# Kernel optimization log

Measured on AMD Instinct MI355X. Metric: run time of the kernel, lower is better.

## Reference

```python
import jax, jax.numpy as jnp
import numpy as np

EPS = 1e-5
DN = ('NCHW', 'OIHW', 'NCHW')


def ternarize(w):
    """Ternary Weight Network quantization with straight-through estimator.
    delta = 0.7 * mean|w|; alpha = mean of |w| over kept entries.
    """
    aw = jnp.abs(w)
    delta = 0.7 * aw.mean()
    mask = (aw > delta).astype(w.dtype)
    alpha = (aw * mask).sum() / jnp.maximum(mask.sum(), 1.0)
    q = alpha * jnp.sign(w) * mask
    return w + jax.lax.stop_gradient(q - w)


def bn(y, g, b, m, v):
    scale = (g / jnp.sqrt(v + EPS))[None, :, None, None]
    shift = (b - m * g / jnp.sqrt(v + EPS))[None, :, None, None]
    return y * scale + shift


def relu6(y):
    return jnp.clip(y, 0.0, 6.0)


def conv(x, w, stride=1, padding='VALID'):
    return jax.lax.conv_general_dilated(
        x, w, window_strides=(stride, stride), padding=padding,
        dimension_numbers=DN)


def setup_inputs() -> dict:
    key = jax.random.key(0)
    ks = jax.random.split(key, 16)
    inp, oup, expand = 32, 32, 6
    hidden = inp * expand  # 192
    B, H, W = 16, 112, 112
    d = {}
    d['x'] = jax.random.normal(ks[0], (B, inp, H, W), dtype=jnp.float32)
    # 1x1 expand conv
    d['w1'] = jax.random.normal(ks[1], (hidden, inp, 1, 1), dtype=jnp.float32) * 0.1
    d['g1'] = 1.0 + 0.1 * jax.random.normal(ks[2], (hidden,), dtype=jnp.float32)
    d['b1'] = 0.1 * jax.random.normal(ks[3], (hidden,), dtype=jnp.float32)
    d['m1'] = 0.1 * jax.random.normal(ks[4], (hidden,), dtype=jnp.float32)
    d['v1'] = jax.random.uniform(ks[5], (hidden,), minval=0.5, maxval=1.5, dtype=jnp.float32)
    # 3x3 dense conv (no groups in the source -> dense, not depthwise)
    d['w2'] = jax.random.normal(ks[6], (hidden, hidden, 3, 3), dtype=jnp.float32) * 0.05
    d['g2'] = 1.0 + 0.1 * jax.random.normal(ks[7], (hidden,), dtype=jnp.float32)
    d['b2'] = 0.1 * jax.random.normal(ks[8], (hidden,), dtype=jnp.float32)
    d['m2'] = 0.1 * jax.random.normal(ks[9], (hidden,), dtype=jnp.float32)
    d['v2'] = jax.random.uniform(ks[10], (hidden,), minval=0.5, maxval=1.5, dtype=jnp.float32)
    # 1x1 project conv
    d['w3'] = jax.random.normal(ks[11], (oup, hidden, 1, 1), dtype=jnp.float32) * 0.1
    d['g3'] = 1.0 + 0.1 * jax.random.normal(ks[12], (oup,), dtype=jnp.float32)
    d['b3'] = 0.1 * jax.random.normal(ks[13], (oup,), dtype=jnp.float32)
    d['m3'] = 0.1 * jax.random.normal(ks[14], (oup,), dtype=jnp.float32)
    d['v3'] = jax.random.uniform(ks[15], (oup,), minval=0.5, maxval=1.5, dtype=jnp.float32)
    return d


def reference(x, w1, g1, b1, m1, v1, w2, g2, b2, m2, v2, w3, g3, b3, m3, v3):
    # expand: 1x1 ternary conv -> BN -> ReLU6
    h = relu6(bn(conv(x, ternarize(w1)), g1, b1, m1, v1))
    # 3x3 ternary conv (stride=1, padding=1) -> BN -> ReLU6
    h = relu6(bn(conv(h, ternarize(w2), stride=1, padding=((1, 1), (1, 1))), g2, b2, m2, v2))
    # project: 1x1 ternary conv -> BN (no activation)
    h = bn(conv(h, ternarize(w3)), g3, b3, m3, v3)
    # residual connection (stride==1 and inp==oup)
    return x + h
```

## Files before the change

kernel.cpp:

```cpp
#include <hip/hip_runtime.h>


typedef __bf16 bf16x8 __attribute__((ext_vector_type(8)));
typedef __bf16 bf16x4 __attribute__((ext_vector_type(4)));
typedef float  f32x4  __attribute__((ext_vector_type(4)));

#define EPSBN 1e-5f

__device__ __forceinline__ void glds16(const void* g, void* l) {
  __builtin_amdgcn_global_load_lds(
      (const __attribute__((address_space(1))) void*)g,
      (__attribute__((address_space(3))) void*)l, 16, 0, 0);
}

__device__ __forceinline__ __bf16 tern(float w, float delta) {
  float aw = fabsf(w);
  float q = (aw > delta) ? ((w > 0.0f) ? 1.0f : -1.0f) : 0.0f;
  return (__bf16)q;
}


__global__ void stats_pass1(const float* __restrict__ w1, const float* __restrict__ w2,
                            const float* __restrict__ w3, double* __restrict__ pa) {
  __shared__ double red[256];
  int b = blockIdx.x, tid = threadIdx.x;
  int tix = b >> 5, slice = b & 31;
  const float* w = (tix == 0) ? w1 : (tix == 1) ? w2 : w3;
  int len = (tix == 1) ? 331776 : 6144;
  int per = len >> 5;
  int start = slice * per, end = start + per;
  double s = 0.0;
  for (int i = start + tid; i < end; i += 256) s += (double)fabsf(w[i]);
  red[tid] = s; __syncthreads();
  for (int off = 128; off > 0; off >>= 1) {
    if (tid < off) red[tid] += red[tid + off];
    __syncthreads();
  }
  if (tid == 0) pa[b] = red[0];
}

__global__ void stats_pass2(const float* __restrict__ w1, const float* __restrict__ w2,
                            const float* __restrict__ w3, const double* __restrict__ pa,
                            double* __restrict__ ps2, double* __restrict__ pc2) {
  __shared__ double red[256];
  int b = blockIdx.x, tid = threadIdx.x;
  int tix = b >> 5, slice = b & 31;
  const float* w = (tix == 0) ? w1 : (tix == 1) ? w2 : w3;
  int len = (tix == 1) ? 331776 : 6144;
  double tot = 0.0;
  for (int k = 0; k < 32; ++k) tot += pa[tix * 32 + k];
  float delta = 0.7f * (float)(tot / (double)len);
  int per = len >> 5;
  int start = slice * per, end = start + per;
  double s2 = 0.0, c2 = 0.0;
  for (int i = start + tid; i < end; i += 256) {
    float aw = fabsf(w[i]);
    if (aw > delta) { s2 += (double)aw; c2 += 1.0; }
  }
  red[tid] = s2; __syncthreads();
  for (int off = 128; off > 0; off >>= 1) {
    if (tid < off) red[tid] += red[tid + off];
    __syncthreads();
  }
  if (tid == 0) ps2[b] = red[0];
  __syncthreads();
  red[tid] = c2; __syncthreads();
  for (int off = 128; off > 0; off >>= 1) {
    if (tid < off) red[tid] += red[tid + off];
    __syncthreads();
  }
  if (tid == 0) pc2[b] = red[0];
}

__global__ void stats_pass3(const double* __restrict__ pa, const double* __restrict__ ps2,
                            const double* __restrict__ pc2, float* __restrict__ stats) {
  int tix = blockIdx.x;
  if (threadIdx.x != 0) return;
  double tot = 0.0, s2 = 0.0, c2 = 0.0;
  for (int k = 0; k < 32; ++k) {
    tot += pa[tix * 32 + k];
    s2  += ps2[tix * 32 + k];
    c2  += pc2[tix * 32 + k];
  }
  int len = (tix == 1) ? 331776 : 6144;
  stats[tix * 2]     = 0.7f * (float)(tot / (double)len);
  stats[tix * 2 + 1] = (float)(s2 / fmax(c2, 1.0));
}

__global__ void pack_kernel(
    const float* __restrict__ w1, const float* __restrict__ w2, const float* __restrict__ w3,
    const float* __restrict__ g1, const float* __restrict__ b1, const float* __restrict__ m1, const float* __restrict__ v1,
    const float* __restrict__ g2, const float* __restrict__ b2, const float* __restrict__ m2, const float* __restrict__ v2,
    const float* __restrict__ g3, const float* __restrict__ b3, const float* __restrict__ m3, const float* __restrict__ v3,
    const float* __restrict__ stats,
    __bf16* __restrict__ w1p, __bf16* __restrict__ w2p, __bf16* __restrict__ w3p,
    float* __restrict__ sc1, float* __restrict__ sh1,
    float* __restrict__ sc2, float* __restrict__ sh2,
    float* __restrict__ sc3, float* __restrict__ sh3) {
  int idx = blockIdx.x * 256 + threadIdx.x;
  if (idx < 331776) {
    float delta2 = stats[2];
    int c = idx / 6144, rem = idx - c * 6144;
    int co = rem >> 5, r5 = rem & 31;
    int cp = r5 >> 3, lo = r5 & 7;
    int tap = c / 6, cb = c - tap * 6;
    int ci = ((cp ^ ((co >> 2) & 3)) << 3) | lo;
    int cifull = cb * 32 + ci;
    w2p[idx] = tern(w2[(co * 192 + cifull) * 9 + tap], delta2);
    return;
  }
  idx -= 331776;
  if (idx < 6144) {
    int co = idx >> 5, c = (idx >> 3) & 3, lo = idx & 7;
    int ci = ((c ^ ((co >> 2) & 3)) << 3) | lo;
    w1p[idx] = tern(w1[co * 32 + ci], stats[0]);
    return;
  }
  idx -= 6144;
  if (idx < 6144) {
    int kc = idx >> 11, rem = idx & 2047;
    int co = rem >> 6, c = (rem >> 3) & 7, lo = rem & 7;
    int ci = ((c ^ (co & 7)) << 3) | lo;
    w3p[idx] = tern(w3[co * 192 + kc * 64 + ci], stats[4]);
    return;
  }
  idx -= 6144;
  if (idx < 192) {
    float rs = rsqrtf(v1[idx] + EPSBN);
    sc1[idx] = g1[idx] * rs * stats[1];
    sh1[idx] = b1[idx] - m1[idx] * g1[idx] * rs;
    return;
  }
  idx -= 192;
  if (idx < 192) {
    float rs = rsqrtf(v2[idx] + EPSBN);
    sc2[idx] = g2[idx] * rs * stats[3];
    sh2[idx] = b2[idx] - m2[idx] * g2[idx] * rs;
    return;
  }
  idx -= 192;
  if (idx < 32) {
    float rs = rsqrtf(v3[idx] + EPSBN);
    sc3[idx] = g3[idx] * rs * stats[5];
    sh3[idx] = b3[idx] - m3[idx] * g3[idx] * rs;
  }
}

__global__ __launch_bounds__(256)
void conv1_kernel(const float* __restrict__ x, const __bf16* __restrict__ w1p,
                  const float* __restrict__ scale1, const float* __restrict__ shift1,
                  __bf16* __restrict__ h1p) {
  __shared__ __bf16 smA[112 * 32];
  __shared__ __bf16 smB[192 * 32];
  int tid = threadIdx.x, lane = tid & 63, wave = tid >> 6;
  int h = blockIdx.x, n = blockIdx.y;

  for (int t = wave; t < 12; t += 4)
    glds16((const char*)w1p + t * 1024 + lane * 16, (char*)smB + t * 1024);

  const float* xrow = x + (long)n * 401408 + h * 112;
  for (int i = 0; i < 14; ++i) {
    int f = i * 256 + tid;
    int ci = f / 112, w = f - ci * 112;
    int col = ((ci >> 3) ^ ((w >> 2) & 3));
    smA[w * 32 + (col << 3) + (ci & 7)] = (__bf16)xrow[ci * 12544 + w];
  }
  __syncthreads();

  int mrow = lane & 15, quad = lane >> 4;
  int col16 = (quad ^ ((mrow >> 2) & 3)) * 16;
  int c0 = wave * 48;

  bf16x8 aw[3], bv[7];
#pragma unroll
  for (int ic = 0; ic < 3; ++ic)
    aw[ic] = *(const bf16x8*)((const char*)smB + (c0 + ic * 16 + mrow) * 64 + col16);
#pragma unroll
  for (int jp = 0; jp < 7; ++jp)
    bv[jp] = *(const bf16x8*)((const char*)smA + (jp * 16 + mrow) * 64 + col16);

  f32x4 acc[7][3];
#pragma unroll
  for (int jp = 0; jp < 7; ++jp)
#pragma unroll
    for (int ic = 0; ic < 3; ++ic) acc[jp][ic] = (f32x4)0.0f;

#pragma unroll
  for (int jp = 0; jp < 7; ++jp)
#pragma unroll
    for (int ic = 0; ic < 3; ++ic)
      acc[jp][ic] = __builtin_amdgcn_mfma_f32_16x16x32_bf16(aw[ic], bv[jp], acc[jp][ic], 0, 0, 0);

  __bf16* obase = h1p + ((long)(n * 114 + h + 1) * 114 + 1) * 192;
#pragma unroll
  for (int ic = 0; ic < 3; ++ic) {
    int co0 = c0 + ic * 16 + quad * 4;
    float4 sc = *(const float4*)(scale1 + co0);
    float4 sh = *(const float4*)(shift1 + co0);
#pragma unroll
    for (int jp = 0; jp < 7; ++jp) {
      int w = jp * 16 + mrow;
      bf16x4 o;
      o[0] = (__bf16)fminf(fmaxf(acc[jp][ic][0] * sc.x + sh.x, 0.0f), 6.0f);
      o[1] = (__bf16)fminf(fmaxf(acc[jp][ic][1] * sc.y + sh.y, 0.0f), 6.0f);
      o[2] = (__bf16)fminf(fmaxf(acc[jp][ic][2] * sc.z + sh.z, 0.0f), 6.0f);
      o[3] = (__bf16)fminf(fmaxf(acc[jp][ic][3] * sc.w + sh.w, 0.0f), 6.0f);
      *(bf16x4*)(obase + w * 192 + co0) = o;
    }
  }

  float4 z = make_float4(0.f, 0.f, 0.f, 0.f);
  if (tid < 48) {
    int px = (tid < 24) ? 0 : 113;
    int c8 = (tid < 24) ? tid : tid - 24;
    *(float4*)((char*)h1p + ((long)((n * 114 + h + 1) * 114 + px) * 384) + c8 * 16) = z;
  }
  if (h == 0) {
    for (int c = tid; c < 2736; c += 256)
      *(float4*)((char*)h1p + (long)(n * 114) * 114 * 384 + c * 16) = z;
  }
  if (h == 111) {
    for (int c = tid; c < 2736; c += 256)
      *(float4*)((char*)h1p + (long)(n * 114 + 113) * 114 * 384 + c * 16) = z;
  }
}


#define STAGE_W(TAP, CB, B) do {                                              \
  _Pragma("unroll")                                                           \
  for (int it_ = 0; it_ < 3; ++it_) {                                         \
    int t_ = wave + it_ * 4;                                                  \
    glds16(w2b + (long)((TAP) * 6 + (CB)) * 12288 + t_ * 1024 + lane * 16,    \
           smBb + (B) * 12288 + t_ * 1024);                                   \
  }                                                                           \
} while (0)

#define STAGE_A(CB) do {                                                      \
  _Pragma("unroll")                                                           \
  for (int it_ = 0; it_ < 8; ++it_)                                           \
    if (aoff[it_] >= 0)                                                       \
      glds16(h1b + aoff[it_] + (CB) * 64, smAb + (wave + it_ * 4) * 1024);    \
} while (0)

__global__ __launch_bounds__(256, 2)
void conv2_kernel(const __bf16* __restrict__ h1p, const __bf16* __restrict__ w2p,
                  const float* __restrict__ scale2, const float* __restrict__ shift2,
                  const __bf16* __restrict__ w3p,
                  const float* __restrict__ scale3, const float* __restrict__ shift3,
                  const float* __restrict__ x, float* __restrict__ out) {
  __shared__ __align__(16) char smem[78336];
  char* smAb = smem;
  char* smBb = smem + 29184;
  char* Pb   = smem;
  char* w3l  = smem + 43008;
  int tid = threadIdx.x, lane = tid & 63, wave = tid >> 6;
  int bh = blockIdx.x, n = blockIdx.y;
  int h0 = bh * 2;

  int aoff[8];
#pragma unroll
  for (int it = 0; it < 8; ++it) {
    int t = wave + it * 4;
    int s = t * 64 + lane;
    if (s < 1824) {
      int q = s >> 2, c = s & 3;
      int q_log = c ^ ((q >> 2) & 3);
      int prow = q / 114, pcol = q - prow * 114;
      aoff[it] = ((n * 114 + h0 + prow) * 114 + pcol) * 384 + q_log * 16;
    } else {
      aoff[it] = -1;
    }
  }

  int pg = wave >> 1, cg = wave & 1;
  int mrow = lane & 15, quad = lane >> 4;
  int col16 = (quad ^ ((mrow >> 2) & 3)) * 16;
  const char* h1b = (const char*)h1p;
  const char* w2b = (const char*)w2p;

  f32x4 acc[7][6];
#pragma unroll
  for (int jp = 0; jp < 7; ++jp)
#pragma unroll
    for (int ic = 0; ic < 6; ++ic) acc[jp][ic] = (f32x4)0.0f;

  STAGE_A(0);
  STAGE_W(0, 0, 0);
  STAGE_W(1, 0, 1);

  for (int cb = 0; cb < 6; ++cb) {
#pragma unroll
    for (int tap = 0; tap < 9; ++tap) {
      if (tap <= 6) {
        STAGE_W(tap + 2, cb, (tap + 2) & 3);
        asm volatile("s_waitcnt vmcnt(6)" ::: "memory");
      } else if (tap == 7) {
        asm volatile("s_waitcnt vmcnt(3)" ::: "memory");
      } else {
        asm volatile("s_waitcnt vmcnt(0)" ::: "memory");
      }
      __builtin_amdgcn_s_barrier();
      __builtin_amdgcn_sched_barrier(0);

      const char* bbuf = smBb + (tap & 3) * 12288;
      bf16x8 aw[6];
#pragma unroll
      for (int ic = 0; ic < 6; ++ic)
        aw[ic] = *(const bf16x8*)(bbuf + (cg * 96 + ic * 16 + mrow) * 64 + col16);

      int dy = tap / 3, dx = tap - dy * 3;
      int base = (pg + dy) * 114 + dx;
      __builtin_amdgcn_s_setprio(1);
#pragma unroll
      for (int jp = 0; jp < 7; ++jp) {
        int row = base + jp * 16 + mrow;
        bf16x8 av = *(const bf16x8*)(smAb + row * 64 +
                                     ((quad ^ ((row >> 2) & 3)) * 16));
#pragma unroll
        for (int ic = 0; ic < 6; ++ic)
          acc[jp][ic] = __builtin_amdgcn_mfma_f32_16x16x32_bf16(aw[ic], av, acc[jp][ic], 0, 0, 0);
      }
      __builtin_amdgcn_s_setprio(0);
    }

    if (cb < 5) {
      asm volatile("s_waitcnt lgkmcnt(0)" ::: "memory");
      __builtin_amdgcn_sched_barrier(0);
      __builtin_amdgcn_s_barrier();
      STAGE_A(cb + 1);
      STAGE_W(0, cb + 1, 0);
      STAGE_W(1, cb + 1, 1);
    }
  }

  asm volatile("s_waitcnt lgkmcnt(0)" ::: "memory");
  __builtin_amdgcn_s_barrier();
  __builtin_amdgcn_sched_barrier(0);

#pragma unroll
  for (int it = 0; it < 3; ++it) {
    int t = wave + it * 4;
    glds16((const char*)w3p + t * 1024 + lane * 16, w3l + t * 1024);
  }

  int cohalf = wave & 1;
  int co3 = cohalf * 16 + mrow;
  float sc3v = scale3[co3], sh3v = shift3[co3];
  int fbase = (wave >> 1) * 4;

#pragma unroll
  for (int rg = 0; rg < 2; ++rg) {
    if (pg == rg) {
#pragma unroll
      for (int ic = 0; ic < 6; ++ic) {
        int co0 = cg * 96 + ic * 16 + quad * 4;
        float4 sc = *(const float4*)(scale2 + co0);
        float4 sh = *(const float4*)(shift2 + co0);
        int kc = co0 >> 6, c6 = co0 & 63;
        int chunk = c6 >> 3, off = c6 & 7;
#pragma unroll
        for (int jp = 0; jp < 7; ++jp) {
          int px = jp * 16 + mrow;
          bf16x4 o;
          o[0] = (__bf16)fminf(fmaxf(acc[jp][ic][0] * sc.x + sh.x, 0.0f), 6.0f);
          o[1] = (__bf16)fminf(fmaxf(acc[jp][ic][1] * sc.y + sh.y, 0.0f), 6.0f);
          o[2] = (__bf16)fminf(fmaxf(acc[jp][ic][2] * sc.z + sh.z, 0.0f), 6.0f);
          o[3] = (__bf16)fminf(fmaxf(acc[jp][ic][3] * sc.w + sh.w, 0.0f), 6.0f);
          *(bf16x4*)(Pb + px * 384 + kc * 128 + ((chunk ^ (px & 7)) * 16) + off * 2) = o;
        }
      }
    }
    if (rg == 0)
      asm volatile("s_waitcnt vmcnt(0) lgkmcnt(0)" ::: "memory");
    else
      asm volatile("s_waitcnt lgkmcnt(0)" ::: "memory");
    __builtin_amdgcn_s_barrier();
    __builtin_amdgcn_sched_barrier(0);

    f32x4 acc3[4];
#pragma unroll
    for (int f = 0; f < 4; ++f) acc3[f] = (f32x4)0.0f;
    int swz = mrow & 7;
#pragma unroll
    for (int kc = 0; kc < 3; ++kc) {
      bf16x8 b0 = *(const bf16x8*)(w3l + kc * 4096 + (cohalf * 16 + mrow) * 128 +
                                   ((quad ^ swz) * 16));
      bf16x8 b1 = *(const bf16x8*)(w3l + kc * 4096 + (cohalf * 16 + mrow) * 128 +
                                   (((4 + quad) ^ swz) * 16));
#pragma unroll
      for (int f = 0; f < 4; ++f) {
        if (fbase + f < 7) {
          int pr = (fbase + f) * 16 + mrow;
          bf16x8 a0 = *(const bf16x8*)(Pb + pr * 384 + kc * 128 + ((quad ^ swz) * 16));
          bf16x8 a1 = *(const bf16x8*)(Pb + pr * 384 + kc * 128 + (((4 + quad) ^ swz) * 16));
          acc3[f] = __builtin_amdgcn_mfma_f32_16x16x32_bf16(a0, b0, acc3[f], 0, 0, 0);
          acc3[f] = __builtin_amdgcn_mfma_f32_16x16x32_bf16(a1, b1, acc3[f], 0, 0, 0);
        }
      }
    }
    int h = h0 + rg;
    long obase = ((long)(n * 32 + co3) * 112 + h) * 112;
    const float* xb = x + obase;
    float* ob = out + obase;
#pragma unroll
    for (int f = 0; f < 4; ++f) {
      if (fbase + f < 7) {
        int w0 = (fbase + f) * 16 + quad * 4;
        float4 xv = *(const float4*)(xb + w0);
        float4 o;
        o.x = acc3[f][0] * sc3v + sh3v + xv.x;
        o.y = acc3[f][1] * sc3v + sh3v + xv.y;
        o.z = acc3[f][2] * sc3v + sh3v + xv.z;
        o.w = acc3[f][3] * sc3v + sh3v + xv.w;
        *(float4*)(ob + w0) = o;
      }
    }
    if (rg == 0) {
      asm volatile("s_waitcnt lgkmcnt(0)" ::: "memory");
      __builtin_amdgcn_s_barrier();
      __builtin_amdgcn_sched_barrier(0);
    }
  }
}

extern "C" void kernel_launch(void* const* d_in, const int* in_sizes, int n_in,
                              void* d_out, int out_size, void* d_ws, size_t ws_size,
                              hipStream_t stream) {
  const float* x  = (const float*)d_in[0];
  const float* w1 = (const float*)d_in[1];
  const float* g1 = (const float*)d_in[2];
  const float* b1 = (const float*)d_in[3];
  const float* m1 = (const float*)d_in[4];
  const float* v1 = (const float*)d_in[5];
  const float* w2 = (const float*)d_in[6];
  const float* g2 = (const float*)d_in[7];
  const float* b2 = (const float*)d_in[8];
  const float* m2 = (const float*)d_in[9];
  const float* v2 = (const float*)d_in[10];
  const float* w3 = (const float*)d_in[11];
  const float* g3 = (const float*)d_in[12];
  const float* b3 = (const float*)d_in[13];
  const float* m3 = (const float*)d_in[14];
  const float* v3 = (const float*)d_in[15];
  float* out = (float*)d_out;

  char* ws = (char*)d_ws;
  float*  stats = (float*)ws;
  double* pa    = (double*)(ws + 256);
  double* ps2   = (double*)(ws + 1024);
  double* pc2   = (double*)(ws + 1792);
  float* sc1 = (float*)(ws + 2560);
  float* sh1 = (float*)(ws + 3328);
  float* sc2 = (float*)(ws + 4096);
  float* sh2 = (float*)(ws + 4864);
  float* sc3 = (float*)(ws + 5632);
  float* sh3 = (float*)(ws + 5760);
  __bf16* w1p = (__bf16*)(ws + 8192);
  __bf16* w3p = (__bf16*)(ws + 20480);
  __bf16* w2p = (__bf16*)(ws + 32768);
  __bf16* h1p = (__bf16*)(ws + (1 << 20));

  hipLaunchKernelGGL(stats_pass1, dim3(96), dim3(256), 0, stream, w1, w2, w3, pa);
  hipLaunchKernelGGL(stats_pass2, dim3(96), dim3(256), 0, stream, w1, w2, w3, pa, ps2, pc2);
  hipLaunchKernelGGL(stats_pass3, dim3(3), dim3(64), 0, stream, pa, ps2, pc2, stats);
  hipLaunchKernelGGL(pack_kernel, dim3(1346), dim3(256), 0, stream, w1, w2, w3,
                     g1, b1, m1, v1, g2, b2, m2, v2, g3, b3, m3, v3, stats,
                     w1p, w2p, w3p, sc1, sh1, sc2, sh2, sc3, sh3);
  hipLaunchKernelGGL(conv1_kernel, dim3(112, 16), dim3(256), 0, stream, x, w1p, sc1, sh1, h1p);
  hipLaunchKernelGGL(conv2_kernel, dim3(56, 16), dim3(256), 0, stream, h1p, w2p, sc2, sh2,
                     w3p, sc3, sh3, x, out);
}
```

Measured before the change: 267.1 us.

## Fuse expand conv into 3x3 conv kernel, recomputing halo rows in LDS

```diff
diff --git a/kernel.cpp b/kernel.cpp
--- a/kernel.cpp
+++ b/kernel.cpp
@@ -6,6 +6,13 @@
 typedef float  f32x4  __attribute__((ext_vector_type(4)));
 
 #define EPSBN 1e-5f
+
+#define XB_OFF   0
+#define W1L_OFF  43008
+#define SMA_OFF  55296
+#define SMB_OFF  99072
+#define SC1_OFF  148224
+#define SH1_OFF  148992
 
 __device__ __forceinline__ void glds16(const void* g, void* l) {
   __builtin_amdgcn_global_load_lds(
@@ -72,34 +79,34 @@
   if (tid == 0) pc2[b] = red[0];
 }
 
-__global__ void stats_pass3(const double* __restrict__ pa, const double* __restrict__ ps2,
-                            const double* __restrict__ pc2, float* __restrict__ stats) {
-  int tix = blockIdx.x;
-  if (threadIdx.x != 0) return;
-  double tot = 0.0, s2 = 0.0, c2 = 0.0;
-  for (int k = 0; k < 32; ++k) {
-    tot += pa[tix * 32 + k];
-    s2  += ps2[tix * 32 + k];
-    c2  += pc2[tix * 32 + k];
-  }
-  int len = (tix == 1) ? 331776 : 6144;
-  stats[tix * 2]     = 0.7f * (float)(tot / (double)len);
-  stats[tix * 2 + 1] = (float)(s2 / fmax(c2, 1.0));
-}
-
 __global__ void pack_kernel(
     const float* __restrict__ w1, const float* __restrict__ w2, const float* __restrict__ w3,
     const float* __restrict__ g1, const float* __restrict__ b1, const float* __restrict__ m1, const float* __restrict__ v1,
     const float* __restrict__ g2, const float* __restrict__ b2, const float* __restrict__ m2, const float* __restrict__ v2,
     const float* __restrict__ g3, const float* __restrict__ b3, const float* __restrict__ m3, const float* __restrict__ v3,
-    const float* __restrict__ stats,
+    const double* __restrict__ pa, const double* __restrict__ ps2, const double* __restrict__ pc2,
     __bf16* __restrict__ w1p, __bf16* __restrict__ w2p, __bf16* __restrict__ w3p,
     float* __restrict__ sc1, float* __restrict__ sh1,
     float* __restrict__ sc2, float* __restrict__ sh2,
     float* __restrict__ sc3, float* __restrict__ sh3) {
-  int idx = blockIdx.x * 256 + threadIdx.x;
+  __shared__ float sst[6];
+  int tid = threadIdx.x;
+  if (tid < 3) {
+    double tot = 0.0, s2 = 0.0, c2 = 0.0;
+    for (int k = 0; k < 32; ++k) {
+      tot += pa[tid * 32 + k];
+      s2  += ps2[tid * 32 + k];
+      c2  += pc2[tid * 32 + k];
+    }
+    int len = (tid == 1) ? 331776 : 6144;
+    sst[tid * 2]     = 0.7f * (float)(tot / (double)len);
+    sst[tid * 2 + 1] = (float)(s2 / fmax(c2, 1.0));
+  }
+  __syncthreads();
+
+  int idx = blockIdx.x * 256 + tid;
   if (idx < 331776) {
-    float delta2 = stats[2];
+    float delta2 = sst[2];
     int c = idx / 6144, rem = idx - c * 6144;
     int co = rem >> 5, r5 = rem & 31;
     int cp = r5 >> 3, lo = r5 & 7;
@@ -113,7 +120,7 @@
   if (idx < 6144) {
     int co = idx >> 5, c = (idx >> 3) & 3, lo = idx & 7;
     int ci = ((c ^ ((co >> 2) & 3)) << 3) | lo;
-    w1p[idx] = tern(w1[co * 32 + ci], stats[0]);
+    w1p[idx] = tern(w1[co * 32 + ci], sst[0]);
     return;
   }
   idx -= 6144;
@@ -121,188 +128,158 @@
     int kc = idx >> 11, rem = idx & 2047;
     int co = rem >> 6, c = (rem >> 3) & 7, lo = rem & 7;
     int ci = ((c ^ (co & 7)) << 3) | lo;
-    w3p[idx] = tern(w3[co * 192 + kc * 64 + ci], stats[4]);
+    w3p[idx] = tern(w3[co * 192 + kc * 64 + ci], sst[4]);
     return;
   }
   idx -= 6144;
   if (idx < 192) {
     float rs = rsqrtf(v1[idx] + EPSBN);
-    sc1[idx] = g1[idx] * rs * stats[1];
+    sc1[idx] = g1[idx] * rs * sst[1];
     sh1[idx] = b1[idx] - m1[idx] * g1[idx] * rs;
     return;
   }
   idx -= 192;
   if (idx < 192) {
     float rs = rsqrtf(v2[idx] + EPSBN);
-    sc2[idx] = g2[idx] * rs * stats[3];
+    sc2[idx] = g2[idx] * rs * sst[3];
     sh2[idx] = b2[idx] - m2[idx] * g2[idx] * rs;
     return;
   }
   idx -= 192;
   if (idx < 32) {
     float rs = rsqrtf(v3[idx] + EPSBN);
-    sc3[idx] = g3[idx] * rs * stats[5];
+    sc3[idx] = g3[idx] * rs * sst[5];
     sh3[idx] = b3[idx] - m3[idx] * g3[idx] * rs;
-  }
-}
-
-__global__ __launch_bounds__(256)
-void conv1_kernel(const float* __restrict__ x, const __bf16* __restrict__ w1p,
-                  const float* __restrict__ scale1, const float* __restrict__ shift1,
-                  __bf16* __restrict__ h1p) {
-  __shared__ __bf16 smA[112 * 32];
-  __shared__ __bf16 smB[192 * 32];
-  int tid = threadIdx.x, lane = tid & 63, wave = tid >> 6;
-  int h = blockIdx.x, n = blockIdx.y;
-
-  for (int t = wave; t < 12; t += 4)
-    glds16((const char*)w1p + t * 1024 + lane * 16, (char*)smB + t * 1024);
-
-  const float* xrow = x + (long)n * 401408 + h * 112;
-  for (int i = 0; i < 14; ++i) {
-    int f = i * 256 + tid;
-    int ci = f / 112, w = f - ci * 112;
-    int col = ((ci >> 3) ^ ((w >> 2) & 3));
-    smA[w * 32 + (col << 3) + (ci & 7)] = (__bf16)xrow[ci * 12544 + w];
-  }
-  __syncthreads();
-
-  int mrow = lane & 15, quad = lane >> 4;
-  int col16 = (quad ^ ((mrow >> 2) & 3)) * 16;
-  int c0 = wave * 48;
-
-  bf16x8 aw[3], bv[7];
-#pragma unroll
-  for (int ic = 0; ic < 3; ++ic)
-    aw[ic] = *(const bf16x8*)((const char*)smB + (c0 + ic * 16 + mrow) * 64 + col16);
-#pragma unroll
-  for (int jp = 0; jp < 7; ++jp)
-    bv[jp] = *(const bf16x8*)((const char*)smA + (jp * 16 + mrow) * 64 + col16);
-
-  f32x4 acc[7][3];
-#pragma unroll
-  for (int jp = 0; jp < 7; ++jp)
-#pragma unroll
-    for (int ic = 0; ic < 3; ++ic) acc[jp][ic] = (f32x4)0.0f;
-
-#pragma unroll
-  for (int jp = 0; jp < 7; ++jp)
-#pragma unroll
-    for (int ic = 0; ic < 3; ++ic)
-      acc[jp][ic] = __builtin_amdgcn_mfma_f32_16x16x32_bf16(aw[ic], bv[jp], acc[jp][ic], 0, 0, 0);
-
-  __bf16* obase = h1p + ((long)(n * 114 + h + 1) * 114 + 1) * 192;
-#pragma unroll
-  for (int ic = 0; ic < 3; ++ic) {
-    int co0 = c0 + ic * 16 + quad * 4;
-    float4 sc = *(const float4*)(scale1 + co0);
-    float4 sh = *(const float4*)(shift1 + co0);
-#pragma unroll
-    for (int jp = 0; jp < 7; ++jp) {
-      int w = jp * 16 + mrow;
-      bf16x4 o;
-      o[0] = (__bf16)fminf(fmaxf(acc[jp][ic][0] * sc.x + sh.x, 0.0f), 6.0f);
-      o[1] = (__bf16)fminf(fmaxf(acc[jp][ic][1] * sc.y + sh.y, 0.0f), 6.0f);
-      o[2] = (__bf16)fminf(fmaxf(acc[jp][ic][2] * sc.z + sh.z, 0.0f), 6.0f);
-      o[3] = (__bf16)fminf(fmaxf(acc[jp][ic][3] * sc.w + sh.w, 0.0f), 6.0f);
-      *(bf16x4*)(obase + w * 192 + co0) = o;
-    }
-  }
-
-  float4 z = make_float4(0.f, 0.f, 0.f, 0.f);
-  if (tid < 48) {
-    int px = (tid < 24) ? 0 : 113;
-    int c8 = (tid < 24) ? tid : tid - 24;
-    *(float4*)((char*)h1p + ((long)((n * 114 + h + 1) * 114 + px) * 384) + c8 * 16) = z;
-  }
-  if (h == 0) {
-    for (int c = tid; c < 2736; c += 256)
-      *(float4*)((char*)h1p + (long)(n * 114) * 114 * 384 + c * 16) = z;
-  }
-  if (h == 111) {
-    for (int c = tid; c < 2736; c += 256)
-      *(float4*)((char*)h1p + (long)(n * 114 + 113) * 114 * 384 + c * 16) = z;
   }
 }
 
 
 #define STAGE_W(TAP, CB, B) do {                                              \
   _Pragma("unroll")                                                           \
-  for (int it_ = 0; it_ < 3; ++it_) {                                         \
-    int t_ = wave + it_ * 4;                                                  \
-    glds16(w2b + (long)((TAP) * 6 + (CB)) * 12288 + t_ * 1024 + lane * 16,    \
-           smBb + (B) * 12288 + t_ * 1024);                                   \
+  for (int it_ = 0; it_ < 2; ++it_) {                                         \
+    int t_ = wave + it_ * 8;                                                  \
+    if (t_ < 12)                                                              \
+      glds16(w2b + (long)((TAP) * 6 + (CB)) * 12288 + t_ * 1024 + lane * 16,  \
+             smem + SMB_OFF + (B) * 12288 + t_ * 1024);                       \
   }                                                                           \
 } while (0)
 
-#define STAGE_A(CB) do {                                                      \
+#define CONV1_PHASE(CB) do {                                                  \
+  int co0_ = (CB) * 32 + cg * 16 + quad * 4;                                  \
+  float4 sc_ = *(const float4*)(smem + SC1_OFF + co0_ * 4);                   \
+  float4 sh_ = *(const float4*)(smem + SH1_OFF + co0_ * 4);                   \
+  bf16x8 aw1_ = *(const bf16x8*)(smem + W1L_OFF +                             \
+                                 ((CB) * 32 + cg * 16 + mrow) * 64 + col16);  \
   _Pragma("unroll")                                                           \
-  for (int it_ = 0; it_ < 8; ++it_)                                           \
-    if (aoff[it_] >= 0)                                                       \
-      glds16(h1b + aoff[it_] + (CB) * 64, smAb + (wave + it_ * 4) * 1024);    \
+  for (int k_ = 0; k_ < 11; ++k_) {                                           \
+    int pf_ = pg + k_ * 4;                                                    \
+    if (pf_ < 42) {                                                           \
+      int r_ = pf_ / 7;                                                       \
+      int xr_ = h0 - 1 + r_;                                                  \
+      if (xr_ >= 0 && xr_ < 112) {                                            \
+        bf16x8 bx_ = *(const bf16x8*)(smem + XB_OFF +                         \
+                                      (pf_ * 16 + mrow) * 64 + col16);        \
+        f32x4 a1_ = __builtin_amdgcn_mfma_f32_16x16x32_bf16(                  \
+            aw1_, bx_, (f32x4)0.0f, 0, 0, 0);                                 \
+        int wcol_ = (pf_ - r_ * 7) * 16 + mrow;                               \
+        int srow_ = r_ * 114 + wcol_ + 1;                                     \
+        bf16x4 o_;                                                            \
+        o_[0] = (__bf16)fminf(fmaxf(a1_[0] * sc_.x + sh_.x, 0.0f), 6.0f);     \
+        o_[1] = (__bf16)fminf(fmaxf(a1_[1] * sc_.y + sh_.y, 0.0f), 6.0f);     \
+        o_[2] = (__bf16)fminf(fmaxf(a1_[2] * sc_.z + sh_.z, 0.0f), 6.0f);     \
+        o_[3] = (__bf16)fminf(fmaxf(a1_[3] * sc_.w + sh_.w, 0.0f), 6.0f);     \
+        int chk_ = ((cg * 2 + (quad >> 1)) ^ ((srow_ >> 2) & 3)) << 4;        \
+        *(bf16x4*)(smem + SMA_OFF + srow_ * 64 + chk_ + (quad & 1) * 8) = o_; \
+      }                                                                       \
+    }                                                                         \
+  }                                                                           \
 } while (0)
 
-__global__ __launch_bounds__(256, 2)
-void conv2_kernel(const __bf16* __restrict__ h1p, const __bf16* __restrict__ w2p,
+__global__ __launch_bounds__(512, 2)
+void fused_kernel(const float* __restrict__ x, const __bf16* __restrict__ w1p,
+                  const float* __restrict__ sc1g, const float* __restrict__ sh1g,
+                  const __bf16* __restrict__ w2p,
                   const float* __restrict__ scale2, const float* __restrict__ shift2,
                   const __bf16* __restrict__ w3p,
                   const float* __restrict__ scale3, const float* __restrict__ shift3,
-                  const float* __restrict__ x, float* __restrict__ out) {
-  __shared__ __align__(16) char smem[78336];
-  char* smAb = smem;
-  char* smBb = smem + 29184;
-  char* Pb   = smem;
-  char* w3l  = smem + 43008;
+                  float* __restrict__ out) {
+  __shared__ __align__(16) char smem[149760];
   int tid = threadIdx.x, lane = tid & 63, wave = tid >> 6;
   int bh = blockIdx.x, n = blockIdx.y;
-  int h0 = bh * 2;
-
-  int aoff[8];
-#pragma unroll
-  for (int it = 0; it < 8; ++it) {
-    int t = wave + it * 4;
-    int s = t * 64 + lane;
-    if (s < 1824) {
-      int q = s >> 2, c = s & 3;
-      int q_log = c ^ ((q >> 2) & 3);
-      int prow = q / 114, pcol = q - prow * 114;
-      aoff[it] = ((n * 114 + h0 + prow) * 114 + pcol) * 384 + q_log * 16;
-    } else {
-      aoff[it] = -1;
-    }
-  }
-
+  int h0 = bh * 4;
   int pg = wave >> 1, cg = wave & 1;
   int mrow = lane & 15, quad = lane >> 4;
   int col16 = (quad ^ ((mrow >> 2) & 3)) * 16;
-  const char* h1b = (const char*)h1p;
   const char* w2b = (const char*)w2p;
 
+  for (int t = tid; t < 2736; t += 512)
+    *(float4*)(smem + SMA_OFF + t * 16) = make_float4(0.f, 0.f, 0.f, 0.f);
+
+#pragma unroll
+  for (int it = 0; it < 2; ++it) {
+    int t = wave + it * 8;
+    if (t < 12)
+      glds16((const char*)w1p + t * 1024 + lane * 16, smem + W1L_OFF + t * 1024);
+  }
+  if (tid < 192) {
+    *(float*)(smem + SC1_OFF + tid * 4) = sc1g[tid];
+    *(float*)(smem + SH1_OFF + tid * 4) = sh1g[tid];
+  }
+  {
+    const float* xn = x + (long)n * 401408;
+    for (int i = 0; i < 11; ++i) {
+      int f4 = i * 512 + tid;
+      if (f4 < 5376) {
+        int ci = f4 / 168, rem = f4 - ci * 168;
+        int px0 = rem * 4;
+        int r = px0 / 112, w0 = px0 - r * 112;
+        int xr = h0 - 1 + r;
+        if (xr >= 0 && xr < 112) {
+          float4 v = *(const float4*)(xn + (ci * 112 + xr) * 112 + w0);
+          int chunk = ((ci >> 3) ^ ((px0 >> 2) & 3)) << 4;
+          char* base = smem + XB_OFF + px0 * 64 + chunk + (ci & 7) * 2;
+          *(__bf16*)(base)       = (__bf16)v.x;
+          *(__bf16*)(base + 64)  = (__bf16)v.y;
+          *(__bf16*)(base + 128) = (__bf16)v.z;
+          *(__bf16*)(base + 192) = (__bf16)v.w;
+        }
+      }
+    }
+  }
+  asm volatile("s_waitcnt vmcnt(0) lgkmcnt(0)" ::: "memory");
+  __builtin_amdgcn_s_barrier();
+  __builtin_amdgcn_sched_barrier(0);
+
   f32x4 acc[7][6];
 #pragma unroll
   for (int jp = 0; jp < 7; ++jp)
 #pragma unroll
     for (int ic = 0; ic < 6; ++ic) acc[jp][ic] = (f32x4)0.0f;
 
-  STAGE_A(0);
   STAGE_W(0, 0, 0);
   STAGE_W(1, 0, 1);
+  CONV1_PHASE(0);
+  asm volatile("s_waitcnt lgkmcnt(0)" ::: "memory");
+  __builtin_amdgcn_s_barrier();
+  __builtin_amdgcn_sched_barrier(0);
 
   for (int cb = 0; cb < 6; ++cb) {
 #pragma unroll
     for (int tap = 0; tap < 9; ++tap) {
       if (tap <= 6) {
         STAGE_W(tap + 2, cb, (tap + 2) & 3);
-        asm volatile("s_waitcnt vmcnt(6)" ::: "memory");
+        if (wave < 4) asm volatile("s_waitcnt vmcnt(4)" ::: "memory");
+        else          asm volatile("s_waitcnt vmcnt(2)" ::: "memory");
       } else if (tap == 7) {
-        asm volatile("s_waitcnt vmcnt(3)" ::: "memory");
+        if (wave < 4) asm volatile("s_waitcnt vmcnt(2)" ::: "memory");
+        else          asm volatile("s_waitcnt vmcnt(1)" ::: "memory");
       } else {
         asm volatile("s_waitcnt vmcnt(0)" ::: "memory");
       }
       __builtin_amdgcn_s_barrier();
       __builtin_amdgcn_sched_barrier(0);
 
-      const char* bbuf = smBb + (tap & 3) * 12288;
+      const char* bbuf = smem + SMB_OFF + (tap & 3) * 12288;
       bf16x8 aw[6];
 #pragma unroll
       for (int ic = 0; ic < 6; ++ic)
@@ -314,7 +291,7 @@
 #pragma unroll
       for (int jp = 0; jp < 7; ++jp) {
         int row = base + jp * 16 + mrow;
-        bf16x8 av = *(const bf16x8*)(smAb + row * 64 +
+        bf16x8 av = *(const bf16x8*)(smem + SMA_OFF + row * 64 +
                                      ((quad ^ ((row >> 2) & 3)) * 16));
 #pragma unroll
         for (int ic = 0; ic < 6; ++ic)
@@ -327,9 +304,12 @@
       asm volatile("s_waitcnt lgkmcnt(0)" ::: "memory");
       __builtin_amdgcn_sched_barrier(0);
       __builtin_amdgcn_s_barrier();
-      STAGE_A(cb + 1);
       STAGE_W(0, cb + 1, 0);
       STAGE_W(1, cb + 1, 1);
+      CONV1_PHASE(cb + 1);
+      asm volatile("s_waitcnt lgkmcnt(0)" ::: "memory");
+      __builtin_amdgcn_s_barrier();
+      __builtin_amdgcn_sched_barrier(0);
     }
   }
 
@@ -338,18 +318,17 @@
   __builtin_amdgcn_sched_barrier(0);
 
 #pragma unroll
-  for (int it = 0; it < 3; ++it) {
-    int t = wave + it * 4;
-    glds16((const char*)w3p + t * 1024 + lane * 16, w3l + t * 1024);
-  }
-
-  int cohalf = wave & 1;
-  int co3 = cohalf * 16 + mrow;
+  for (int it = 0; it < 2; ++it) {
+    int t = wave + it * 8;
+    if (t < 12)
+      glds16((const char*)w3p + t * 1024 + lane * 16, smem + W1L_OFF + t * 1024);
+  }
+
+  int co3 = cg * 16 + mrow;
   float sc3v = scale3[co3], sh3v = shift3[co3];
-  int fbase = (wave >> 1) * 4;
-
-#pragma unroll
-  for (int rg = 0; rg < 2; ++rg) {
+
+#pragma unroll
+  for (int rg = 0; rg < 4; ++rg) {
     if (pg == rg) {
 #pragma unroll
       for (int ic = 0; ic < 6; ++ic) {
@@ -366,7 +345,8 @@
           o[1] = (__bf16)fminf(fmaxf(acc[jp][ic][1] * sc.y + sh.y, 0.0f), 6.0f);
           o[2] = (__bf16)fminf(fmaxf(acc[jp][ic][2] * sc.z + sh.z, 0.0f), 6.0f);
           o[3] = (__bf16)fminf(fmaxf(acc[jp][ic][3] * sc.w + sh.w, 0.0f), 6.0f);
-          *(bf16x4*)(Pb + px * 384 + kc * 128 + ((chunk ^ (px & 7)) * 16) + off * 2) = o;
+          *(bf16x4*)(smem + XB_OFF + px * 384 + kc * 128 +
+                     ((chunk ^ (px & 7)) * 16) + off * 2) = o;
         }
       }
     }
@@ -377,24 +357,26 @@
     __builtin_amdgcn_s_barrier();
     __builtin_amdgcn_sched_barrier(0);
 
-    f32x4 acc3[4];
-#pragma unroll
-    for (int f = 0; f < 4; ++f) acc3[f] = (f32x4)0.0f;
+    f32x4 acc3[2];
+    acc3[0] = (f32x4)0.0f; acc3[1] = (f32x4)0.0f;
     int swz = mrow & 7;
 #pragma unroll
     for (int kc = 0; kc < 3; ++kc) {
-      bf16x8 b0 = *(const bf16x8*)(w3l + kc * 4096 + (cohalf * 16 + mrow) * 128 +
-                                   ((quad ^ swz) * 16));
-      bf16x8 b1 = *(const bf16x8*)(w3l + kc * 4096 + (cohalf * 16 + mrow) * 128 +
-                                   (((4 + quad) ^ swz) * 16));
-#pragma unroll
-      for (int f = 0; f < 4; ++f) {
-        if (fbase + f < 7) {
-          int pr = (fbase + f) * 16 + mrow;
-          bf16x8 a0 = *(const bf16x8*)(Pb + pr * 384 + kc * 128 + ((quad ^ swz) * 16));
-          bf16x8 a1 = *(const bf16x8*)(Pb + pr * 384 + kc * 128 + (((4 + quad) ^ swz) * 16));
-          acc3[f] = __builtin_amdgcn_mfma_f32_16x16x32_bf16(a0, b0, acc3[f], 0, 0, 0);
-          acc3[f] = __builtin_amdgcn_mfma_f32_16x16x32_bf16(a1, b1, acc3[f], 0, 0, 0);
+      bf16x8 b0 = *(const bf16x8*)(smem + W1L_OFF + kc * 4096 +
+                                   (cg * 16 + mrow) * 128 + ((quad ^ swz) * 16));
+      bf16x8 b1 = *(const bf16x8*)(smem + W1L_OFF + kc * 4096 +
+                                   (cg * 16 + mrow) * 128 + (((4 + quad) ^ swz) * 16));
+#pragma unroll
+      for (int f2 = 0; f2 < 2; ++f2) {
+        int f = pg * 2 + f2;
+        if (f < 7) {
+          int pr = f * 16 + mrow;
+          bf16x8 a0 = *(const bf16x8*)(smem + XB_OFF + pr * 384 + kc * 128 +
+                                       ((quad ^ swz) * 16));
+          bf16x8 a1 = *(const bf16x8*)(smem + XB_OFF + pr * 384 + kc * 128 +
+                                       (((4 + quad) ^ swz) * 16));
+          acc3[f2] = __builtin_amdgcn_mfma_f32_16x16x32_bf16(a0, b0, acc3[f2], 0, 0, 0);
+          acc3[f2] = __builtin_amdgcn_mfma_f32_16x16x32_bf16(a1, b1, acc3[f2], 0, 0, 0);
         }
       }
     }
@@ -403,19 +385,20 @@
     const float* xb = x + obase;
     float* ob = out + obase;
 #pragma unroll
-    for (int f = 0; f < 4; ++f) {
-      if (fbase + f < 7) {
-        int w0 = (fbase + f) * 16 + quad * 4;
+    for (int f2 = 0; f2 < 2; ++f2) {
+      int f = pg * 2 + f2;
+      if (f < 7) {
+        int w0 = f * 16 + quad * 4;
         float4 xv = *(const float4*)(xb + w0);
         float4 o;
-        o.x = acc3[f][0] * sc3v + sh3v + xv.x;
-        o.y = acc3[f][1] * sc3v + sh3v + xv.y;
-        o.z = acc3[f][2] * sc3v + sh3v + xv.z;
-        o.w = acc3[f][3] * sc3v + sh3v + xv.w;
+        o.x = acc3[f2][0] * sc3v + sh3v + xv.x;
+        o.y = acc3[f2][1] * sc3v + sh3v + xv.y;
+        o.z = acc3[f2][2] * sc3v + sh3v + xv.z;
+        o.w = acc3[f2][3] * sc3v + sh3v + xv.w;
         *(float4*)(ob + w0) = o;
       }
     }
-    if (rg == 0) {
+    if (rg < 3) {
       asm volatile("s_waitcnt lgkmcnt(0)" ::: "memory");
       __builtin_amdgcn_s_barrier();
       __builtin_amdgcn_sched_barrier(0);
@@ -445,7 +428,6 @@
   float* out = (float*)d_out;
 
   char* ws = (char*)d_ws;
-  float*  stats = (float*)ws;
   double* pa    = (double*)(ws + 256);
   double* ps2   = (double*)(ws + 1024);
   double* pc2   = (double*)(ws + 1792);
@@ -458,15 +440,12 @@
   __bf16* w1p = (__bf16*)(ws + 8192);
   __bf16* w3p = (__bf16*)(ws + 20480);
   __bf16* w2p = (__bf16*)(ws + 32768);
-  __bf16* h1p = (__bf16*)(ws + (1 << 20));
 
   hipLaunchKernelGGL(stats_pass1, dim3(96), dim3(256), 0, stream, w1, w2, w3, pa);
   hipLaunchKernelGGL(stats_pass2, dim3(96), dim3(256), 0, stream, w1, w2, w3, pa, ps2, pc2);
-  hipLaunchKernelGGL(stats_pass3, dim3(3), dim3(64), 0, stream, pa, ps2, pc2, stats);
   hipLaunchKernelGGL(pack_kernel, dim3(1346), dim3(256), 0, stream, w1, w2, w3,
-                     g1, b1, m1, v1, g2, b2, m2, v2, g3, b3, m3, v3, stats,
+                     g1, b1, m1, v1, g2, b2, m2, v2, g3, b3, m3, v3, pa, ps2, pc2,
                      w1p, w2p, w3p, sc1, sh1, sc2, sh2, sc3, sh3);
-  hipLaunchKernelGGL(conv1_kernel, dim3(112, 16), dim3(256), 0, stream, x, w1p, sc1, sh1, h1p);
-  hipLaunchKernelGGL(conv2_kernel, dim3(56, 16), dim3(256), 0, stream, h1p, w2p, sc2, sh2,
-                     w3p, sc3, sh3, x, out);
-}
+  hipLaunchKernelGGL(fused_kernel, dim3(28, 16), dim3(512), 0, stream, x, w1p, sc1, sh1,
+                     w2p, sc2, sh2, w3p, sc3, sh3, out);
+}
```

Measured after the change: 402.3 us. 50.6% more time.

## Fold stats finalize into pack kernel and stage conv1 output through LDS

Applied to the files above, without the earlier changes.

```diff
diff --git a/kernel.cpp b/kernel.cpp
--- a/kernel.cpp
+++ b/kernel.cpp
@@ -72,34 +72,34 @@
   if (tid == 0) pc2[b] = red[0];
 }
 
-__global__ void stats_pass3(const double* __restrict__ pa, const double* __restrict__ ps2,
-                            const double* __restrict__ pc2, float* __restrict__ stats) {
-  int tix = blockIdx.x;
-  if (threadIdx.x != 0) return;
-  double tot = 0.0, s2 = 0.0, c2 = 0.0;
-  for (int k = 0; k < 32; ++k) {
-    tot += pa[tix * 32 + k];
-    s2  += ps2[tix * 32 + k];
-    c2  += pc2[tix * 32 + k];
-  }
-  int len = (tix == 1) ? 331776 : 6144;
-  stats[tix * 2]     = 0.7f * (float)(tot / (double)len);
-  stats[tix * 2 + 1] = (float)(s2 / fmax(c2, 1.0));
-}
-
 __global__ void pack_kernel(
     const float* __restrict__ w1, const float* __restrict__ w2, const float* __restrict__ w3,
     const float* __restrict__ g1, const float* __restrict__ b1, const float* __restrict__ m1, const float* __restrict__ v1,
     const float* __restrict__ g2, const float* __restrict__ b2, const float* __restrict__ m2, const float* __restrict__ v2,
     const float* __restrict__ g3, const float* __restrict__ b3, const float* __restrict__ m3, const float* __restrict__ v3,
-    const float* __restrict__ stats,
+    const double* __restrict__ pa, const double* __restrict__ ps2, const double* __restrict__ pc2,
     __bf16* __restrict__ w1p, __bf16* __restrict__ w2p, __bf16* __restrict__ w3p,
     float* __restrict__ sc1, float* __restrict__ sh1,
     float* __restrict__ sc2, float* __restrict__ sh2,
     float* __restrict__ sc3, float* __restrict__ sh3) {
-  int idx = blockIdx.x * 256 + threadIdx.x;
+  __shared__ float sst[6];
+  int tid = threadIdx.x;
+  if (tid < 3) {
+    double tot = 0.0, s2 = 0.0, c2 = 0.0;
+    for (int k = 0; k < 32; ++k) {
+      tot += pa[tid * 32 + k];
+      s2  += ps2[tid * 32 + k];
+      c2  += pc2[tid * 32 + k];
+    }
+    int len = (tid == 1) ? 331776 : 6144;
+    sst[tid * 2]     = 0.7f * (float)(tot / (double)len);
+    sst[tid * 2 + 1] = (float)(s2 / fmax(c2, 1.0));
+  }
+  __syncthreads();
+
+  int idx = blockIdx.x * 256 + tid;
   if (idx < 331776) {
-    float delta2 = stats[2];
+    float delta2 = sst[2];
     int c = idx / 6144, rem = idx - c * 6144;
     int co = rem >> 5, r5 = rem & 31;
     int cp = r5 >> 3, lo = r5 & 7;
@@ -113,7 +113,7 @@
   if (idx < 6144) {
     int co = idx >> 5, c = (idx >> 3) & 3, lo = idx & 7;
     int ci = ((c ^ ((co >> 2) & 3)) << 3) | lo;
-    w1p[idx] = tern(w1[co * 32 + ci], stats[0]);
+    w1p[idx] = tern(w1[co * 32 + ci], sst[0]);
     return;
   }
   idx -= 6144;
@@ -121,27 +121,27 @@
     int kc = idx >> 11, rem = idx & 2047;
     int co = rem >> 6, c = (rem >> 3) & 7, lo = rem & 7;
     int ci = ((c ^ (co & 7)) << 3) | lo;
-    w3p[idx] = tern(w3[co * 192 + kc * 64 + ci], stats[4]);
+    w3p[idx] = tern(w3[co * 192 + kc * 64 + ci], sst[4]);
     return;
   }
   idx -= 6144;
   if (idx < 192) {
     float rs = rsqrtf(v1[idx] + EPSBN);
-    sc1[idx] = g1[idx] * rs * stats[1];
+    sc1[idx] = g1[idx] * rs * sst[1];
     sh1[idx] = b1[idx] - m1[idx] * g1[idx] * rs;
     return;
   }
   idx -= 192;
   if (idx < 192) {
     float rs = rsqrtf(v2[idx] + EPSBN);
-    sc2[idx] = g2[idx] * rs * stats[3];
+    sc2[idx] = g2[idx] * rs * sst[3];
     sh2[idx] = b2[idx] - m2[idx] * g2[idx] * rs;
     return;
   }
   idx -= 192;
   if (idx < 32) {
     float rs = rsqrtf(v3[idx] + EPSBN);
-    sc3[idx] = g3[idx] * rs * stats[5];
+    sc3[idx] = g3[idx] * rs * sst[5];
     sh3[idx] = b3[idx] - m3[idx] * g3[idx] * rs;
   }
 }
@@ -150,20 +150,31 @@
 void conv1_kernel(const float* __restrict__ x, const __bf16* __restrict__ w1p,
                   const float* __restrict__ scale1, const float* __restrict__ shift1,
                   __bf16* __restrict__ h1p) {
-  __shared__ __bf16 smA[112 * 32];
-  __shared__ __bf16 smB[192 * 32];
+  __shared__ __align__(16) char smem[57344];
+  char* smA = smem;
+  char* smB = smem + 7168;
+  char* Pb  = smem;
   int tid = threadIdx.x, lane = tid & 63, wave = tid >> 6;
   int h = blockIdx.x, n = blockIdx.y;
 
   for (int t = wave; t < 12; t += 4)
-    glds16((const char*)w1p + t * 1024 + lane * 16, (char*)smB + t * 1024);
+    glds16((const char*)w1p + t * 1024 + lane * 16, smB + t * 1024);
 
   const float* xrow = x + (long)n * 401408 + h * 112;
-  for (int i = 0; i < 14; ++i) {
-    int f = i * 256 + tid;
-    int ci = f / 112, w = f - ci * 112;
-    int col = ((ci >> 3) ^ ((w >> 2) & 3));
-    smA[w * 32 + (col << 3) + (ci & 7)] = (__bf16)xrow[ci * 12544 + w];
+#pragma unroll
+  for (int i = 0; i < 4; ++i) {
+    int g = i * 256 + tid;
+    if (g < 896) {
+      int ci0 = (g / 112) * 4, w = g - (g / 112) * 112;
+      const float* p = xrow + ci0 * 12544 + w;
+      bf16x4 v;
+      v[0] = (__bf16)p[0];
+      v[1] = (__bf16)p[12544];
+      v[2] = (__bf16)p[25088];
+      v[3] = (__bf16)p[37632];
+      int col = ((ci0 >> 3) ^ ((w >> 2) & 3));
+      *(bf16x4*)(smA + w * 64 + (col << 4) + (ci0 & 7) * 2) = v;
+    }
   }
   __syncthreads();
 
@@ -174,10 +185,14 @@
   bf16x8 aw[3], bv[7];
 #pragma unroll
   for (int ic = 0; ic < 3; ++ic)
-    aw[ic] = *(const bf16x8*)((const char*)smB + (c0 + ic * 16 + mrow) * 64 + col16);
+    aw[ic] = *(const bf16x8*)(smB + (c0 + ic * 16 + mrow) * 64 + col16);
 #pragma unroll
   for (int jp = 0; jp < 7; ++jp)
-    bv[jp] = *(const bf16x8*)((const char*)smA + (jp * 16 + mrow) * 64 + col16);
+    bv[jp] = *(const bf16x8*)(smA + (jp * 16 + mrow) * 64 + col16);
+
+  asm volatile("s_waitcnt lgkmcnt(0)" ::: "memory");
+  __builtin_amdgcn_s_barrier();
+  __builtin_amdgcn_sched_barrier(0);
 
   f32x4 acc[7][3];
 #pragma unroll
@@ -191,12 +206,13 @@
     for (int ic = 0; ic < 3; ++ic)
       acc[jp][ic] = __builtin_amdgcn_mfma_f32_16x16x32_bf16(aw[ic], bv[jp], acc[jp][ic], 0, 0, 0);
 
-  __bf16* obase = h1p + ((long)(n * 114 + h + 1) * 114 + 1) * 192;
 #pragma unroll
   for (int ic = 0; ic < 3; ++ic) {
     int co0 = c0 + ic * 16 + quad * 4;
     float4 sc = *(const float4*)(scale1 + co0);
     float4 sh = *(const float4*)(shift1 + co0);
+    int lch = co0 >> 3;
+    int boff = (quad & 1) * 8;
 #pragma unroll
     for (int jp = 0; jp < 7; ++jp) {
       int w = jp * 16 + mrow;
@@ -205,7 +221,21 @@
       o[1] = (__bf16)fminf(fmaxf(acc[jp][ic][1] * sc.y + sh.y, 0.0f), 6.0f);
       o[2] = (__bf16)fminf(fmaxf(acc[jp][ic][2] * sc.z + sh.z, 0.0f), 6.0f);
       o[3] = (__bf16)fminf(fmaxf(acc[jp][ic][3] * sc.w + sh.w, 0.0f), 6.0f);
-      *(bf16x4*)(obase + w * 192 + co0) = o;
+      *(bf16x4*)(Pb + w * 512 + ((lch ^ (w & 31)) << 4) + boff) = o;
+    }
+  }
+  asm volatile("s_waitcnt lgkmcnt(0)" ::: "memory");
+  __builtin_amdgcn_s_barrier();
+  __builtin_amdgcn_sched_barrier(0);
+
+  __bf16* obase = h1p + ((long)(n * 114 + h + 1) * 114 + 1) * 192;
+#pragma unroll
+  for (int i = 0; i < 11; ++i) {
+    int c = i * 256 + tid;
+    if (c < 2688) {
+      int w = c / 24, lch = c - w * 24;
+      float4 v = *(const float4*)(Pb + w * 512 + ((lch ^ (w & 31)) << 4));
+      *(float4*)((char*)obase + c * 16) = v;
     }
   }
 
@@ -445,7 +475,6 @@
   float* out = (float*)d_out;
 
   char* ws = (char*)d_ws;
-  float*  stats = (float*)ws;
   double* pa    = (double*)(ws + 256);
   double* ps2   = (double*)(ws + 1024);
   double* pc2   = (double*)(ws + 1792);
@@ -462,9 +491,8 @@
 
   hipLaunchKernelGGL(stats_pass1, dim3(96), dim3(256), 0, stream, w1, w2, w3, pa);
   hipLaunchKernelGGL(stats_pass2, dim3(96), dim3(256), 0, stream, w1, w2, w3, pa, ps2, pc2);
-  hipLaunchKernelGGL(stats_pass3, dim3(3), dim3(64), 0, stream, pa, ps2, pc2, stats);
   hipLaunchKernelGGL(pack_kernel, dim3(1346), dim3(256), 0, stream, w1, w2, w3,
-                     g1, b1, m1, v1, g2, b2, m2, v2, g3, b3, m3, v3, stats,
+                     g1, b1, m1, v1, g2, b2, m2, v2, g3, b3, m3, v3, pa, ps2, pc2,
                      w1p, w2p, w3p, sc1, sh1, sc2, sh2, sc3, sh3);
   hipLaunchKernelGGL(conv1_kernel, dim3(112, 16), dim3(256), 0, stream, x, w1p, sc1, sh1, h1p);
   hipLaunchKernelGGL(conv2_kernel, dim3(56, 16), dim3(256), 0, stream, h1p, w2p, sc2, sh2,
```

Result: faster. 261.4 us (-2.1%).
